# Performance work log

Hardware: AMD Instinct MI355X
Metric: run time of the kernel (lower is better)

## Reference

```python
import jax, jax.numpy as jnp
import numpy as np

B, V, E = 8, 12288, 98304   # batch, nodes (healpix nside=32), edges (~8 nbrs/node)
FIN, FOUT, K = 256, 256, 4  # channels, Chebyshev order
EPS = 1e-5                  # BatchNorm1d eps


def setup_inputs() -> dict:
    key = jax.random.key(0)
    ks = jax.random.split(key, 5)
    x = jax.random.normal(ks[0], (B, V, FIN), jnp.float32)
    edge_src = jax.random.randint(ks[1], (E,), 0, V, dtype=jnp.int32)
    edge_dst = jax.random.randint(ks[2], (E,), 0, V, dtype=jnp.int32)
    edge_weight = jax.random.normal(ks[3], (E,), jnp.float32) * 0.3
    scale = (2.0 / (FIN * K)) ** 0.5  # kaiming-style init over K*Fin fan-in
    weight = jax.random.normal(ks[4], (K, FIN, FOUT), jnp.float32) * scale
    bias = jnp.zeros((FOUT,), jnp.float32)
    gamma = jnp.ones((FOUT,), jnp.float32)
    beta = jnp.zeros((FOUT,), jnp.float32)
    return {"x": x, "edge_weight": edge_weight, "weight": weight, "bias": bias,
            "gamma": gamma, "beta": beta, "edge_src": edge_src, "edge_dst": edge_dst}


def reference(x, edge_weight, weight, bias, gamma, beta, edge_src, edge_dst):
    # --- ConvCheb: Chebyshev polynomial recursion over sparse Laplacian ---
    xt = x.transpose(1, 0, 2)  # [V, B, Fin] (node-major for segment scatter)

    def lmul(y):  # sparse L @ y, y: [V, B, Fin]
        msg = edge_weight[:, None, None] * y[edge_src]          # [E, B, Fin]
        return jax.ops.segment_sum(msg, edge_dst, num_segments=V)

    xs = [xt]                                  # T_0(L) x = x
    if K > 1:
        xs.append(lmul(xt))                    # T_1(L) x = L x
    for _ in range(2, K):
        xs.append(2.0 * lmul(xs[-1]) - xs[-2])  # T_k = 2 L T_{k-1} - T_{k-2}
    xk = jnp.stack(xs)                         # [K, V, B, Fin]

    out = jnp.einsum('kvbi,kio->bvo', xk, weight) + bias  # [B, V, Fout]

    # --- BatchNorm1d over channels (training-mode batch stats over B,V) ---
    mean = out.mean(axis=(0, 1))
    var = out.var(axis=(0, 1))  # biased variance, as torch uses for normalization
    out = gamma * (out - mean) * jax.lax.rsqrt(var + EPS) + beta

    return jax.nn.relu(out)
```

## Files before the change

kernel.cpp:

```cpp
#include <hip/hip_runtime.h>

#define Vn    12288
#define En    98304
#define Mrows 98304

typedef unsigned short u16;
typedef u16   u16x8  __attribute__((ext_vector_type(8)));
typedef __bf16 bf16x8 __attribute__((ext_vector_type(8)));
typedef float f32x4  __attribute__((ext_vector_type(4)));

struct __align__(8) Edge { int s; float w; };

__device__ __forceinline__ float bf2f(u16 u) {
    union { float f; unsigned int i; } c; c.i = ((unsigned int)u) << 16; return c.f;
}
__device__ __forceinline__ u16 f2bf(float f) {
    union { float f; unsigned int i; } c; c.f = f;
    unsigned int r = c.i + 0x7fffu + ((c.i >> 16) & 1u);
    return (u16)(r >> 16);
}
__device__ __forceinline__ void load_lds16(const void* g, void* l) {
    __builtin_amdgcn_global_load_lds(
        (const __attribute__((address_space(1))) void*)g,
        (__attribute__((address_space(3))) void*)l, 16, 0, 0);
}

__global__ void cvt_k(const float* __restrict__ x, u16* __restrict__ xb) {
    int v = blockIdx.x;
    int t = threadIdx.x;
    int b = t >> 5, i = (t & 31) * 8;
    const float* p = x + ((size_t)b * Vn + v) * 256 + i;
    f32x4 a0 = *(const f32x4*)p;
    f32x4 a1 = *(const f32x4*)(p + 4);
    u16x8 r;
    #pragma unroll
    for (int j = 0; j < 4; ++j) { r[j] = f2bf(a0[j]); r[4 + j] = f2bf(a1[j]); }
    *(u16x8*)(xb + (size_t)v * 2048 + b * 256 + i) = r;
}

__global__ void wtrans_k(const float* __restrict__ w, u16* __restrict__ wt) {
    int kk = blockIdx.x;
    int o  = threadIdx.x;
    wt[(size_t)o * 1024 + kk] = f2bf(w[(size_t)kk * 256 + o]);
}

__global__ void count_k(const int* __restrict__ dst, int* __restrict__ counts) {
    int e = blockIdx.x * 256 + threadIdx.x;
    atomicAdd(&counts[dst[e]], 1);
}

__global__ void scan_k(const int* __restrict__ counts, int* __restrict__ row_start,
                       int* __restrict__ cursor) {
    __shared__ int par[1024];
    int t = threadIdx.x;
    int base = t * 12;
    int s = 0;
    #pragma unroll
    for (int i = 0; i < 12; ++i) s += counts[base + i];
    par[t] = s;
    __syncthreads();
    for (int off = 1; off < 1024; off <<= 1) {
        int v_ = (t >= off) ? par[t - off] : 0;
        __syncthreads();
        par[t] += v_;
        __syncthreads();
    }
    int run = (t == 0) ? 0 : par[t - 1];
    for (int i = 0; i < 12; ++i) {
        row_start[base + i] = run;
        cursor[base + i]    = run;
        run += counts[base + i];
    }
    if (t == 1023) row_start[Vn] = En;
}

__global__ void fill_k(const int* __restrict__ src, const int* __restrict__ dst,
                       const float* __restrict__ ew, int* __restrict__ cursor,
                       Edge* __restrict__ csr) {
    int e = blockIdx.x * 256 + threadIdx.x;
    int d = dst[e];
    int p = atomicAdd(&cursor[d], 1);
    Edge ed; ed.s = src[e]; ed.w = ew[e];
    csr[p] = ed;
}

template<int PREV>
__global__ __launch_bounds__(256)
void lmul_k(const u16* __restrict__ yb, const u16* __restrict__ prevb,
            u16* __restrict__ outb, const int* __restrict__ row_start,
            const Edge* __restrict__ csr)
{
    int slice = blockIdx.x & 7;
    int v     = (blockIdx.x >> 3) * 8 + (threadIdx.x >> 5);
    int t     = threadIdx.x & 31;
    int s0    = row_start[v];
    int cnt   = row_start[v + 1] - s0;
    size_t soff = (size_t)slice * 256 + (size_t)t * 8;
    float acc[8] = {0.f,0.f,0.f,0.f,0.f,0.f,0.f,0.f};
    for (int j0 = 0; j0 < cnt; j0 += 8) {
        int ss[8]; float ww[8];
        #pragma unroll
        for (int u = 0; u < 8; ++u) {
            int j = j0 + u;
            bool ok = j < cnt;
            Edge e = csr[s0 + (ok ? j : 0)];
            ss[u] = e.s; ww[u] = ok ? e.w : 0.f;
        }
        u16x8 g[8];
        #pragma unroll
        for (int u = 0; u < 8; ++u)
            g[u] = *(const u16x8*)(yb + (size_t)ss[u] * 2048 + soff);
        #pragma unroll
        for (int u = 0; u < 8; ++u)
            #pragma unroll
            for (int j8 = 0; j8 < 8; ++j8) acc[j8] += ww[u] * bf2f(g[u][j8]);
    }
    u16x8 r;
    if (PREV) {
        u16x8 pu = *(const u16x8*)(prevb + (size_t)v * 2048 + soff);
        #pragma unroll
        for (int j8 = 0; j8 < 8; ++j8) r[j8] = f2bf(2.0f * acc[j8] - bf2f(pu[j8]));
    } else {
        #pragma unroll
        for (int j8 = 0; j8 < 8; ++j8) r[j8] = f2bf(acc[j8]);
    }
    *(u16x8*)(outb + (size_t)v * 2048 + soff) = r;
}

__global__ __launch_bounds__(512)
void gemm_k(const u16* __restrict__ x0, const u16* __restrict__ x1,
            const u16* __restrict__ x2, const u16* __restrict__ x3,
            const u16* __restrict__ wt, const float* __restrict__ bias,
            float* __restrict__ outp, float* __restrict__ sums, float* __restrict__ sumsq)
{
    alignas(16) __shared__ char lds[49152];
    int tid  = threadIdx.x;
    int wave = tid >> 6;
    int lane = tid & 63;
    int m0   = blockIdx.x * 128;
    int wm   = wave & 1;
    int wn   = wave >> 1;

    f32x4 acc[4][4];
    #pragma unroll
    for (int a = 0; a < 4; ++a)
        #pragma unroll
        for (int b = 0; b < 4; ++b) acc[a][b] = (f32x4){0.f,0.f,0.f,0.f};

    for (int kt = 0; kt < 16; ++kt) {
        int ks = kt >> 2;
        int k0 = (kt & 3) * 64;
        const u16* Ak = (ks == 0) ? x0 : (ks == 1) ? x1 : (ks == 2) ? x2 : x3;
        #pragma unroll
        for (int r = 0; r < 2; ++r) {
            int g  = r * 512 + tid;
            int ml = g >> 3;
            int c  = (g & 7) ^ (ml & 7);
            load_lds16(Ak + ((size_t)(m0 + ml)) * 256 + k0 + c * 8,
                       lds + r * 8192 + wave * 1024);
        }
        #pragma unroll
        for (int r = 0; r < 4; ++r) {
            int g = r * 512 + tid;
            int o = g >> 3;
            int c = (g & 7) ^ (o & 7);
            load_lds16(wt + (size_t)o * 1024 + kt * 64 + c * 8,
                       lds + 16384 + r * 8192 + wave * 1024);
        }
        __syncthreads();
        #pragma unroll
        for (int kstep = 0; kstep < 2; ++kstep) {
            int cidx = kstep * 4 + (lane >> 4);
            int row  = lane & 15;
            bf16x8 af[4], bfr[4];
            #pragma unroll
            for (int mt = 0; mt < 4; ++mt) {
                int m16 = wm * 64 + mt * 16 + row;
                af[mt] = *(const bf16x8*)(lds + (size_t)(m16 * 8 + (cidx ^ (m16 & 7))) * 16);
            }
            #pragma unroll
            for (int nt = 0; nt < 4; ++nt) {
                int ol = wn * 64 + nt * 16 + row;
                bfr[nt] = *(const bf16x8*)(lds + 16384 + (size_t)(ol * 8 + (cidx ^ (ol & 7))) * 16);
            }
            #pragma unroll
            for (int mt = 0; mt < 4; ++mt)
                #pragma unroll
                for (int nt = 0; nt < 4; ++nt)
                    acc[mt][nt] = __builtin_amdgcn_mfma_f32_16x16x32_bf16(
                        af[mt], bfr[nt], acc[mt][nt], 0, 0, 0);
        }
        __syncthreads();
    }
    int crow = lane & 15, quad = lane >> 4;
    #pragma unroll
    for (int nt = 0; nt < 4; ++nt) {
        int o = wn * 64 + nt * 16 + crow;
        float bv = bias[o];
        float ps = 0.f, pq = 0.f;
        #pragma unroll
        for (int mt = 0; mt < 4; ++mt) {
            #pragma unroll
            for (int r = 0; r < 4; ++r) {
                int m = m0 + wm * 64 + mt * 16 + quad * 4 + r;
                float val = acc[mt][nt][r] + bv;
                outp[((size_t)((m & 7) * Vn + (m >> 3))) * 256 + o] = val;
                ps += val; pq += val * val;
            }
        }
        ps += __shfl_down(ps, 32, 64);  pq += __shfl_down(pq, 32, 64);
        ps += __shfl_down(ps, 16, 64);  pq += __shfl_down(pq, 16, 64);
        if (quad == 0) { atomicAdd(&sums[o], ps); atomicAdd(&sumsq[o], pq); }
    }
}

__global__ void finalize_k(const float* __restrict__ sums, const float* __restrict__ sumsq,
                           const float* __restrict__ gamma, const float* __restrict__ beta,
                           float* __restrict__ scale, float* __restrict__ shift) {
    int o = threadIdx.x;
    const float invM = 1.0f / (float)Mrows;
    float mean = sums[o] * invM;
    float var  = sumsq[o] * invM - mean * mean;
    float sc   = gamma[o] * rsqrtf(var + 1e-5f);
    scale[o] = sc;
    shift[o] = beta[o] - mean * sc;
}

__global__ void bn_relu_k(float* __restrict__ outp, const float* __restrict__ scale,
                          const float* __restrict__ shift) {
    __shared__ float ssc[256], ssh[256];
    int t = threadIdx.x;
    ssc[t] = scale[t]; ssh[t] = shift[t];
    __syncthreads();
    size_t idx = ((size_t)blockIdx.x * 256 + t) * 8;
    int o0 = (int)(idx & 255);
    f32x4 a = *(const f32x4*)(outp + idx);
    f32x4 c = *(const f32x4*)(outp + idx + 4);
    #pragma unroll
    for (int i = 0; i < 4; ++i) {
        a[i] = fmaxf(a[i] * ssc[o0 + i]     + ssh[o0 + i],     0.f);
        c[i] = fmaxf(c[i] * ssc[o0 + 4 + i] + ssh[o0 + 4 + i], 0.f);
    }
    *(f32x4*)(outp + idx)     = a;
    *(f32x4*)(outp + idx + 4) = c;
}

extern "C" void kernel_launch(void* const* d_in, const int* in_sizes, int n_in,
                              void* d_out, int out_size, void* d_ws, size_t ws_size,
                              hipStream_t stream) {
    const float* x     = (const float*)d_in[0];
    const float* ew    = (const float*)d_in[1];
    const float* w     = (const float*)d_in[2];
    const float* bias  = (const float*)d_in[3];
    const float* gamma = (const float*)d_in[4];
    const float* beta  = (const float*)d_in[5];
    const int*   esrc  = (const int*)d_in[6];
    const int*   edst  = (const int*)d_in[7];
    float* outp = (float*)d_out;
    char*  ws   = (char*)d_ws;

    u16*   xb        = (u16*)  (ws + 0);
    u16*   x1        = (u16*)  (ws + 50331648);
    u16*   x2        = (u16*)  (ws + 100663296);
    u16*   x3        = (u16*)  (ws + 150994944);
    u16*   wt        = (u16*)  (ws + 201326592);
    Edge*  csr       = (Edge*) (ws + 201850880);
    int*   counts    = (int*)  (ws + 202637312);
    int*   row_start = (int*)  (ws + 202686464);
    int*   cursor    = (int*)  (ws + 202736128);
    float* sums      = (float*)(ws + 202785280);
    float* sumsq     = (float*)(ws + 202786304);
    float* scale     = (float*)(ws + 202787328);
    float* shift     = (float*)(ws + 202788352);

    hipMemsetAsync(counts, 0, 49152, stream);
    hipMemsetAsync(sums, 0, 2048, stream);

    cvt_k<<<Vn, 256, 0, stream>>>(x, xb);
    wtrans_k<<<1024, 256, 0, stream>>>(w, wt);
    count_k<<<384, 256, 0, stream>>>(edst, counts);
    scan_k<<<1, 1024, 0, stream>>>(counts, row_start, cursor);
    fill_k<<<384, 256, 0, stream>>>(esrc, edst, ew, cursor, csr);

    lmul_k<0><<<Vn, 256, 0, stream>>>(xb, nullptr, x1, row_start, csr);
    lmul_k<1><<<Vn, 256, 0, stream>>>(x1, xb,      x2, row_start, csr);
    lmul_k<1><<<Vn, 256, 0, stream>>>(x2, x1,      x3, row_start, csr);

    gemm_k<<<Mrows / 128, 512, 0, stream>>>(xb, x1, x2, x3, wt, bias, outp, sums, sumsq);

    finalize_k<<<1, 256, 0, stream>>>(sums, sumsq, gamma, beta, scale, shift);
    bn_relu_k<<<12288, 256, 0, stream>>>(outp, scale, shift);
}
```

Measured before the change: 474.5 us.

## Triple-buffer GEMM LDS tiles with async prefetch two stages ahead

Replaces the single-buffered load/sync/compute loop in the fused Chebyshev GEMM with a three-stage LDS ring buffer. Tiles are prefetched two iterations ahead using direct-to-LDS loads, synchronized by explicit vmcnt waits and a single barrier per iteration. MFMA sections also get raised wave priority. The aim is to hide global-load latency behind compute, but LDS use grows to 144 KB per block, which limits occupancy to one block per CU.

Measured after the change: 469.9 us. Within noise of the previous version (-1.0%).

```diff
diff --git a/kernel.cpp b/kernel.cpp
--- a/kernel.cpp
+++ b/kernel.cpp
@@ -127,13 +127,36 @@
     *(u16x8*)(outb + (size_t)v * 2048 + soff) = r;
 }
 
+__device__ __forceinline__ void stage_tile(const u16* __restrict__ Ak, int k0,
+                                           const u16* __restrict__ wt, int kt,
+                                           int m0, int tid, int wave,
+                                           char* bufA, char* bufB)
+{
+    #pragma unroll
+    for (int r = 0; r < 2; ++r) {
+        int g  = r * 512 + tid;
+        int ml = g >> 3;
+        int c  = (g & 7) ^ (ml & 7);
+        load_lds16(Ak + ((size_t)(m0 + ml)) * 256 + k0 + c * 8,
+                   bufA + r * 8192 + wave * 1024);
+    }
+    #pragma unroll
+    for (int r = 0; r < 4; ++r) {
+        int g = r * 512 + tid;
+        int o = g >> 3;
+        int c = (g & 7) ^ (o & 7);
+        load_lds16(wt + (size_t)o * 1024 + kt * 64 + c * 8,
+                   bufB + r * 8192 + wave * 1024);
+    }
+}
+
 __global__ __launch_bounds__(512)
 void gemm_k(const u16* __restrict__ x0, const u16* __restrict__ x1,
             const u16* __restrict__ x2, const u16* __restrict__ x3,
             const u16* __restrict__ wt, const float* __restrict__ bias,
             float* __restrict__ outp, float* __restrict__ sums, float* __restrict__ sumsq)
 {
-    alignas(16) __shared__ char lds[49152];
+    alignas(16) __shared__ char lds[147456];
     int tid  = threadIdx.x;
     int wave = tid >> 6;
     int lane = tid & 63;
@@ -147,27 +170,26 @@
         #pragma unroll
         for (int b = 0; b < 4; ++b) acc[a][b] = (f32x4){0.f,0.f,0.f,0.f};
 
-    for (int kt = 0; kt < 16; ++kt) {
-        int ks = kt >> 2;
-        int k0 = (kt & 3) * 64;
-        const u16* Ak = (ks == 0) ? x0 : (ks == 1) ? x1 : (ks == 2) ? x2 : x3;
-        #pragma unroll
-        for (int r = 0; r < 2; ++r) {
-            int g  = r * 512 + tid;
-            int ml = g >> 3;
-            int c  = (g & 7) ^ (ml & 7);
-            load_lds16(Ak + ((size_t)(m0 + ml)) * 256 + k0 + c * 8,
-                       lds + r * 8192 + wave * 1024);
+    stage_tile(x0, 0,  wt, 0, m0, tid, wave, (char*)lds,         (char*)lds + 16384);
+    stage_tile(x0, 64, wt, 1, m0, tid, wave, (char*)lds + 49152, (char*)lds + 49152 + 16384);
+
+    int cb = 0;
+    int pb = 2;
+    for (int t = 0; t < 16; ++t) {
+        if (t < 15) asm volatile("s_waitcnt vmcnt(6) lgkmcnt(0)" ::: "memory");
+        else        asm volatile("s_waitcnt vmcnt(0) lgkmcnt(0)" ::: "memory");
+        __builtin_amdgcn_s_barrier();
+        __builtin_amdgcn_sched_barrier(0);
+        if (t < 14) {
+            int kt = t + 2;
+            int ks = kt >> 2;
+            int k0 = (kt & 3) * 64;
+            const u16* Ak = (ks == 0) ? x0 : (ks == 1) ? x1 : (ks == 2) ? x2 : x3;
+            stage_tile(Ak, k0, wt, kt, m0, tid, wave,
+                       (char*)lds + pb * 49152, (char*)lds + pb * 49152 + 16384);
         }
-        #pragma unroll
-        for (int r = 0; r < 4; ++r) {
-            int g = r * 512 + tid;
-            int o = g >> 3;
-            int c = (g & 7) ^ (o & 7);
-            load_lds16(wt + (size_t)o * 1024 + kt * 64 + c * 8,
-                       lds + 16384 + r * 8192 + wave * 1024);
-        }
-        __syncthreads();
+        const char* Ab = (const char*)lds + cb * 49152;
+        const char* Bb = Ab + 16384;
         #pragma unroll
         for (int kstep = 0; kstep < 2; ++kstep) {
             int cidx = kstep * 4 + (lane >> 4);
@@ -176,22 +198,26 @@
             #pragma unroll
             for (int mt = 0; mt < 4; ++mt) {
                 int m16 = wm * 64 + mt * 16 + row;
-                af[mt] = *(const bf16x8*)(lds + (size_t)(m16 * 8 + (cidx ^ (m16 & 7))) * 16);
+                af[mt] = *(const bf16x8*)(Ab + (size_t)(m16 * 8 + (cidx ^ (m16 & 7))) * 16);
             }
             #pragma unroll
             for (int nt = 0; nt < 4; ++nt) {
                 int ol = wn * 64 + nt * 16 + row;
-                bfr[nt] = *(const bf16x8*)(lds + 16384 + (size_t)(ol * 8 + (cidx ^ (ol & 7))) * 16);
+                bfr[nt] = *(const bf16x8*)(Bb + (size_t)(ol * 8 + (cidx ^ (ol & 7))) * 16);
             }
+            __builtin_amdgcn_s_setprio(1);
             #pragma unroll
             for (int mt = 0; mt < 4; ++mt)
                 #pragma unroll
                 for (int nt = 0; nt < 4; ++nt)
                     acc[mt][nt] = __builtin_amdgcn_mfma_f32_16x16x32_bf16(
                         af[mt], bfr[nt], acc[mt][nt], 0, 0, 0);
+            __builtin_amdgcn_s_setprio(0);
         }
-        __syncthreads();
-    }
+        cb = (cb == 2) ? 0 : cb + 1;
+        pb = (pb == 2) ? 0 : pb + 1;
+    }
+
     int crow = lane & 15, quad = lane >> 4;
     #pragma unroll
     for (int nt = 0; nt < 4; ++nt) {
```
